# Optimization experiments

Hardware: AMD Instinct MI355X
Metric: run time of the kernel (lower is better)

## Reference

```python
import jax, jax.numpy as jnp
import numpy as np

SLOPE_LIM_THETA = 2.0


def _minmod3(a, b, c):
    """minmod over 3 candidates: min|.| when all same sign, else 0 (matches torch aminmax form)."""
    fmin = jnp.minimum(jnp.minimum(a, b), c)
    fmax = jnp.maximum(jnp.maximum(a, b), c)
    return jnp.where(fmin < 0.0, jnp.minimum(fmax, 0.0), fmin)


def setup_inputs() -> dict:
    key = jax.random.key(0)
    k1, k2 = jax.random.split(key)
    B, M, L = 16, 256, 8192  # L = N + 4 ghost-padded length
    rho = jax.random.normal(k1, (B, M, L), dtype=jnp.float32)
    v = jax.random.normal(k2, (B, M, L), dtype=jnp.float32)
    return {"rho": rho, "v": v, "axis": 2, "retain_padding": 0}


def reference(rho, v, axis, retain_padding):
    th = SLOPE_LIM_THETA
    flux = jnp.swapaxes(rho * v, axis, -1)          # [..., L]
    vv = jnp.swapaxes(v, axis, -1)[..., 1:-1]        # [..., L-2]
    # 3-tap slope candidates (equivalent to Conv1d(1,3,3) with the fixed weights)
    c0 = th * (flux[..., 1:-1] - flux[..., :-2])
    c1 = 0.5 * (flux[..., 2:] - flux[..., :-2])
    c2 = th * (flux[..., 2:] - flux[..., 1:-1])
    half_slope = 0.5 * _minmod3(c0, c1, c2)          # [..., L-2]
    flux_minus = flux[..., 2:-1] - half_slope[..., 1:]   # [..., L-3]
    flux_plus = flux[..., 1:-2] + half_slope[..., :-1]   # [..., L-3]
    flux_minus = jnp.where(vv[..., 1:] >= 0.0, 0.0, flux_minus)
    flux_plus = jnp.where(vv[..., :-1] <= 0.0, 0.0, flux_plus)
    flux_minus = flux_minus.at[..., -1].set(0.0)
    flux_plus = flux_plus.at[..., 0].set(0.0)
    flux_net = flux_minus + flux_plus                # [..., L-3]
    main = jnp.swapaxes(-(flux_net[..., 1:] - flux_net[..., :-1]), axis, -1)  # [..., L-4]
    if retain_padding:
        left = jnp.swapaxes(-flux_net[..., 0:1], axis, -1)[..., 0]
        right = jnp.swapaxes(flux_net[..., -1:], axis, -1)[..., 0]
        return (main, left, right)
    return main
```

## Files before the change

kernel.cpp:

```cpp
#include <hip/hip_runtime.h>


#define TH 2.0f

__device__ __forceinline__ float minmod3(float a, float b, float c) {
    float mn = fminf(fminf(a, b), c);
    float mx = fmaxf(fmaxf(a, b), c);
    return (mn < 0.0f) ? fminf(mx, 0.0f) : mn;
}

__global__ __launch_bounds__(256) void advect_kernel(
    const float* __restrict__ rho, const float* __restrict__ v,
    float* __restrict__ out, int L, int OUT, int GPR)
{
    int g = blockIdx.x * blockDim.x + threadIdx.x;
    if (g >= GPR) return;
    long row = blockIdx.y;
    const float* r  = rho + row * L;
    const float* vp = v   + row * L;
    int k0 = g * 4;

    float4 ra = *(const float4*)(r  + k0);
    float4 rb = *(const float4*)(r  + k0 + 4);
    float4 va = *(const float4*)(vp + k0);
    float4 vb = *(const float4*)(vp + k0 + 4);

    float V[8] = {va.x, va.y, va.z, va.w, vb.x, vb.y, vb.z, vb.w};
    float R[8] = {ra.x, ra.y, ra.z, ra.w, rb.x, rb.y, rb.z, rb.w};
    float F[8];
#pragma unroll
    for (int i = 0; i < 8; ++i) F[i] = R[i] * V[i];

    float hs[6];
#pragma unroll
    for (int i = 0; i < 6; ++i) {
        float c0 = TH   * (F[i+1] - F[i]);
        float c1 = 0.5f * (F[i+2] - F[i]);
        float c2 = TH   * (F[i+2] - F[i+1]);
        hs[i] = 0.5f * minmod3(c0, c1, c2);
    }

    float net[5];
#pragma unroll
    for (int j = 0; j < 5; ++j) {
        int gj = k0 + j;
        float fm = (V[j+2] >= 0.0f || gj == OUT) ? 0.0f : (F[j+2] - hs[j+1]);
        float fp = (V[j+1] <= 0.0f || gj == 0)   ? 0.0f : (F[j+1] + hs[j]);
        net[j] = fm + fp;
    }

    float4 o;
    o.x = net[0] - net[1];
    o.y = net[1] - net[2];
    o.z = net[2] - net[3];
    o.w = net[3] - net[4];
    *(float4*)(out + row * OUT + k0) = o;
}

extern "C" void kernel_launch(void* const* d_in, const int* in_sizes, int n_in,
                              void* d_out, int out_size, void* d_ws, size_t ws_size,
                              hipStream_t stream) {
    const float* rho = (const float*)d_in[0];
    const float* v   = (const float*)d_in[1];
    float* out = (float*)d_out;

    const int L    = 8192;
    const int rows = in_sizes[0] / L;
    const int OUT  = L - 4;
    const int GPR  = OUT / 4;

    dim3 block(256);
    dim3 grid((GPR + 255) / 256, rows);
    hipLaunchKernelGGL(advect_kernel, grid, block, 0, stream,
                       rho, v, out, L, OUT, GPR);
}
```

Baseline: 308.1 us.

## Process sixteen outputs per thread with nontemporal stores and constant sizes

Each thread now computes 16 outputs instead of 4, loading 20 inputs so the halo reread shrinks from 2x to 1.25x of the data per thread. Sizes are compile-time constants, the grid is fixed at 2 blocks per row, and output stores use nontemporal hints. Fewer threads means less parallelism for latency hiding and more registers per thread, and correctness now depends on L being hardcoded to 8192.

```diff
diff --git a/kernel.cpp b/kernel.cpp
--- a/kernel.cpp
+++ b/kernel.cpp
@@ -2,6 +2,8 @@
 
 
 #define TH 2.0f
+
+typedef float floatx4 __attribute__((ext_vector_type(4)));
 
 __device__ __forceinline__ float minmod3(float a, float b, float c) {
     float mn = fminf(fminf(a, b), c);
@@ -11,50 +13,67 @@
 
 __global__ __launch_bounds__(256) void advect_kernel(
     const float* __restrict__ rho, const float* __restrict__ v,
-    float* __restrict__ out, int L, int OUT, int GPR)
+    float* __restrict__ out)
 {
-    int g = blockIdx.x * blockDim.x + threadIdx.x;
-    if (g >= GPR) return;
+    const int L = 8192, OUT = 8188;
+    int t = blockIdx.x * blockDim.x + threadIdx.x;
     long row = blockIdx.y;
-    const float* r  = rho + row * L;
-    const float* vp = v   + row * L;
-    int k0 = g * 4;
+    const float* r  = rho + row * (long)L;
+    const float* vp = v   + row * (long)L;
+    int k0 = t * 16;
 
-    float4 ra = *(const float4*)(r  + k0);
-    float4 rb = *(const float4*)(r  + k0 + 4);
-    float4 va = *(const float4*)(vp + k0);
-    float4 vb = *(const float4*)(vp + k0 + 4);
+    float R[20], V[20];
+#pragma unroll
+    for (int s = 0; s < 4; ++s) {
+        floatx4 a = *(const floatx4*)(r + k0 + 4 * s);
+        R[4*s+0] = a.x; R[4*s+1] = a.y; R[4*s+2] = a.z; R[4*s+3] = a.w;
+        floatx4 b = *(const floatx4*)(vp + k0 + 4 * s);
+        V[4*s+0] = b.x; V[4*s+1] = b.y; V[4*s+2] = b.z; V[4*s+3] = b.w;
+    }
+    if (k0 + 16 < L) {
+        floatx4 a = *(const floatx4*)(r + k0 + 16);
+        R[16] = a.x; R[17] = a.y; R[18] = a.z; R[19] = a.w;
+        floatx4 b = *(const floatx4*)(vp + k0 + 16);
+        V[16] = b.x; V[17] = b.y; V[18] = b.z; V[19] = b.w;
+    } else {
+        R[16] = R[17] = R[18] = R[19] = 0.0f;
+        V[16] = V[17] = V[18] = V[19] = 0.0f;
+    }
 
-    float V[8] = {va.x, va.y, va.z, va.w, vb.x, vb.y, vb.z, vb.w};
-    float R[8] = {ra.x, ra.y, ra.z, ra.w, rb.x, rb.y, rb.z, rb.w};
-    float F[8];
+    float F[20];
 #pragma unroll
-    for (int i = 0; i < 8; ++i) F[i] = R[i] * V[i];
+    for (int i = 0; i < 20; ++i) F[i] = R[i] * V[i];
 
-    float hs[6];
+    float hs[18];
 #pragma unroll
-    for (int i = 0; i < 6; ++i) {
+    for (int i = 0; i < 18; ++i) {
         float c0 = TH   * (F[i+1] - F[i]);
         float c1 = 0.5f * (F[i+2] - F[i]);
         float c2 = TH   * (F[i+2] - F[i+1]);
         hs[i] = 0.5f * minmod3(c0, c1, c2);
     }
 
-    float net[5];
+    float net[17];
 #pragma unroll
-    for (int j = 0; j < 5; ++j) {
+    for (int j = 0; j < 17; ++j) {
         int gj = k0 + j;
         float fm = (V[j+2] >= 0.0f || gj == OUT) ? 0.0f : (F[j+2] - hs[j+1]);
         float fp = (V[j+1] <= 0.0f || gj == 0)   ? 0.0f : (F[j+1] + hs[j]);
         net[j] = fm + fp;
     }
 
-    float4 o;
-    o.x = net[0] - net[1];
-    o.y = net[1] - net[2];
-    o.z = net[2] - net[3];
-    o.w = net[3] - net[4];
-    *(float4*)(out + row * OUT + k0) = o;
+    float* op = out + row * (long)OUT + k0;
+#pragma unroll
+    for (int s = 0; s < 4; ++s) {
+        if (k0 + 4 * s + 3 < OUT) {
+            floatx4 o;
+            o.x = net[4*s+0] - net[4*s+1];
+            o.y = net[4*s+1] - net[4*s+2];
+            o.z = net[4*s+2] - net[4*s+3];
+            o.w = net[4*s+3] - net[4*s+4];
+            __builtin_nontemporal_store(o, (floatx4*)(op + 4 * s));
+        }
+    }
 }
 
 extern "C" void kernel_launch(void* const* d_in, const int* in_sizes, int n_in,
@@ -66,11 +85,7 @@
 
     const int L    = 8192;
     const int rows = in_sizes[0] / L;
-    const int OUT  = L - 4;
-    const int GPR  = OUT / 4;
-
     dim3 block(256);
-    dim3 grid((GPR + 255) / 256, rows);
-    hipLaunchKernelGGL(advect_kernel, grid, block, 0, stream,
-                       rho, v, out, L, OUT, GPR);
+    dim3 grid(2, rows);
+    hipLaunchKernelGGL(advect_kernel, grid, block, 0, stream, rho, v, out);
 }
```

Result: slower. 463.8 us (+50.6%).
